# Kernel tuning notes

Measured on AMD Instinct MI355X. Metric: run time of the kernel, lower is better.

Reference implementation:

```python
import jax, jax.numpy as jnp
import numpy as np

BS, L, D, H, DC = 8, 8192, 128, 128, 128
C_CONST = 8.0  # rg-lru temperature constant


def _ln(x):
    # LayerNorm without scale/bias (use_bias=False, use_scale=False)
    m = jnp.mean(x, axis=-1, keepdims=True)
    v = jnp.mean(jnp.square(x - m), axis=-1, keepdims=True)
    return (x - m) * jax.lax.rsqrt(v + 1e-6)


def _affine(c, w, b):
    # Dense(features=1)(c)[:, :, None] -> (bs, 1, 1) broadcast scalar per sequence
    return (c @ w + b)[:, :, None]


def _combine(e1, e2):
    a1, b1 = e1
    a2, b2 = e2
    return (a1 * a2, a2 * b1 + b2)


def _linear_scan(a, b, reverse):
    # h_t = a_t * h_{t-1} + b_t (or h_{t+1} when reverse) along seq axis 1
    _, h = jax.lax.associative_scan(_combine, (a, b), axis=1, reverse=reverse)
    return h


def _forward(x, c, cln1_sw, cln1_sb, cln1_bw, cln1_bb, gate1_w, gate1_b,
             rnn_in_w, rnn_in_b, pos_emb, rnn_wi, rnn_bi, rnn_wr, rnn_br, rnn_a,
             rnn_out_w, rnn_out_b, cln2_sw, cln2_sb, cln2_bw, cln2_bb,
             gate2_w, gate2_b, mlp_w1, mlp_b1, mlp_w2, mlp_b2):
    # --- branch 1: conditioned LN -> bidirectional RG-LRU -> gated residual ---
    h = (1.0 + _affine(c, cln1_sw, cln1_sb)) * _ln(x) + _affine(c, cln1_bw, cln1_bb)
    u = _ln(h) @ rnn_in_w + rnn_in_b + pos_emb[None]          # (bs, L, H)
    gi = jax.nn.sigmoid(u @ rnn_wi + rnn_bi)                   # input gate
    gr = jax.nn.sigmoid(u @ rnn_wr + rnn_br)                   # recurrence gate
    at = jnp.exp(C_CONST * gr * jnp.log(rnn_a))                # a_t = a^(c*r_t)
    bt = jnp.sqrt(1.0 - jnp.square(at)) * (gi * u)
    hf = _linear_scan(at, bt, reverse=False)
    hb = _linear_scan(at, bt, reverse=True)
    r = jnp.concatenate([hf, hb], axis=-1) @ rnn_out_w + rnn_out_b  # (bs, L, D)
    x = x + _affine(c, gate1_w, gate1_b) * r
    # --- branch 2: conditioned LN -> gelu MLP -> gated residual ---
    h = (1.0 + _affine(c, cln2_sw, cln2_sb)) * _ln(x) + _affine(c, cln2_bw, cln2_bb)
    m = jax.nn.gelu(h @ mlp_w1 + mlp_b1) @ mlp_w2 + mlp_b2
    return x + _affine(c, gate2_w, gate2_b) * m


def setup_inputs() -> dict:
    key = jax.random.key(0)
    ks = jax.random.split(key, 30)
    def n(k, shape, s=0.05):
        return (jax.random.normal(k, shape) * s).astype(jnp.float32)
    rnn_a = (0.9 + 0.09 * jax.random.uniform(ks[0], (H,))).astype(jnp.float32)
    return {
        "x": jax.random.normal(ks[1], (BS, L, D), jnp.float32),
        "c": jax.random.normal(ks[2], (BS, DC), jnp.float32),
        "cln1_sw": n(ks[3], (DC, 1)), "cln1_sb": n(ks[4], (1,)),
        "cln1_bw": n(ks[5], (DC, 1)), "cln1_bb": n(ks[6], (1,)),
        "gate1_w": n(ks[7], (DC, 1)), "gate1_b": n(ks[8], (1,)),
        "rnn_in_w": n(ks[9], (D, H), 0.1), "rnn_in_b": n(ks[10], (H,)),
        "pos_emb": n(ks[11], (L, H), 0.02),
        "rnn_wi": n(ks[12], (H, H), 0.1), "rnn_bi": n(ks[13], (H,)),
        "rnn_wr": n(ks[14], (H, H), 0.1), "rnn_br": n(ks[15], (H,)),
        "rnn_a": rnn_a,
        "rnn_out_w": n(ks[16], (2 * H, D), 0.1), "rnn_out_b": n(ks[17], (D,)),
        "cln2_sw": n(ks[18], (DC, 1)), "cln2_sb": n(ks[19], (1,)),
        "cln2_bw": n(ks[20], (DC, 1)), "cln2_bb": n(ks[21], (1,)),
        "gate2_w": n(ks[22], (DC, 1)), "gate2_b": n(ks[23], (1,)),
        "mlp_w1": n(ks[24], (D, 4 * D), 0.1), "mlp_b1": n(ks[25], (4 * D,)),
        "mlp_w2": n(ks[26], (4 * D, D), 0.1), "mlp_b2": n(ks[27], (D,)),
    }


def reference(x, c, cln1_sw, cln1_sb, cln1_bw, cln1_bb, gate1_w, gate1_b,
              rnn_in_w, rnn_in_b, pos_emb, rnn_wi, rnn_bi, rnn_wr, rnn_br, rnn_a,
              rnn_out_w, rnn_out_b, cln2_sw, cln2_sb, cln2_bw, cln2_bb,
              gate2_w, gate2_b, mlp_w1, mlp_b1, mlp_w2, mlp_b2):
    return _forward(x, c, cln1_sw, cln1_sb, cln1_bw, cln1_bb, gate1_w, gate1_b,
                    rnn_in_w, rnn_in_b, pos_emb, rnn_wi, rnn_bi, rnn_wr, rnn_br, rnn_a,
                    rnn_out_w, rnn_out_b, cln2_sw, cln2_sb, cln2_bw, cln2_bb,
                    gate2_w, gate2_b, mlp_w1, mlp_b1, mlp_w2, mlp_b2)
```

## Files before the change

kernel.cpp:

```cpp
#include <hip/hip_runtime.h>
#include <hip/hip_bf16.h>

#define BSZ 8
#define SEQ 8192
#define DIM 128
#define NCH 128
#define CLEN 64

typedef unsigned short u16;
typedef unsigned int u32;
typedef short bf16x8 __attribute__((ext_vector_type(8)));
typedef float f32x4  __attribute__((ext_vector_type(4)));

__device__ __forceinline__ float us2f(u16 w){ union{u32 i;float f;}u; u.i=((u32)w)<<16; return u.f; }
__device__ __forceinline__ u16 f2us(float f){
  __hip_bfloat16 h = __float2bfloat16(f);
  union{ __hip_bfloat16 b; u16 s; }u; u.b=h; return u.s;
}
__device__ __forceinline__ float wred64(float v){
  #pragma unroll
  for (int o=1;o<64;o<<=1) v += __shfl_xor(v,o,64);
  return v;
}
__device__ __forceinline__ float red16(float v){
  v += __shfl_xor(v,1,64); v += __shfl_xor(v,2,64);
  v += __shfl_xor(v,4,64); v += __shfl_xor(v,8,64);
  return v;
}
__device__ __forceinline__ float sigmoidf_(float z){ return 1.f/(1.f+__expf(-z)); }
__device__ __forceinline__ float gelu_tanh(float x){
  float y = 0.7978845608028654f * fmaf(0.044715f*x, x*x, x);
  float e = __expf(2.f*y);
  float th = 1.f - 2.f/(e+1.f);
  return 0.5f*x*(1.f+th);
}
__device__ __forceinline__ void lds_fence(){
  asm volatile("s_waitcnt lgkmcnt(0)" ::: "memory");
  __builtin_amdgcn_sched_barrier(0);
}

__global__ __launch_bounds__(64) void k_aff(
    const float* __restrict__ c,
    const float* w0,const float* w1,const float* w2,const float* w3,const float* w4,const float* w5,
    const float* s0,const float* s1,const float* s2,const float* s3,const float* s4,const float* s5,
    float* __restrict__ aff)
{
  const float* ws[6]={w0,w1,w2,w3,w4,w5};
  const float* bs[6]={s0,s1,s2,s3,s4,s5};
  int l = threadIdx.x;
  for (int b=0;b<BSZ;++b){
    #pragma unroll
    for (int h=0;h<6;++h){
      float v = c[b*128+l]*ws[h][l] + c[b*128+64+l]*ws[h][64+l];
      v = wred64(v);
      if (l==0) aff[b*6+h] = v + bs[h][0];
    }
  }
}

__device__ __forceinline__ void pack_one(const float* __restrict__ W, int N,
                                         u16* __restrict__ out, int fi)
{
  int lane = fi & 63;
  int k2   = (fi >> 6) & 1;
  int cn   = fi >> 7;
  int NB   = N >> 4;
  int n    = cn % NB, c = cn / NB;
  int k0   = c*64 + k2*32 + (lane>>4)*8;
  int col  = n*16 + (lane&15);
  u16* o = out + (size_t)fi*8;
  #pragma unroll
  for (int j=0;j<8;++j) o[j] = f2us(W[(size_t)(k0+j)*N + col]);
}

__global__ __launch_bounds__(256) void k_prep(
    const float* __restrict__ w1, const float* __restrict__ w2, const float* __restrict__ wo,
    const float* __restrict__ win, const float* __restrict__ wi, const float* __restrict__ wr,
    u16* __restrict__ w1t, u16* __restrict__ w2t, u16* __restrict__ wot,
    u16* __restrict__ wint, u16* __restrict__ wit, u16* __restrict__ wrt)
{
  int i = blockIdx.x*256 + threadIdx.x;
  if      (i <  8192) pack_one(w1, 512, w1t, i);
  else if (i < 16384) pack_one(w2, 128, w2t, i-8192);
  else if (i < 20480) pack_one(wo, 128, wot, i-16384);
  else if (i < 22528) pack_one(win,128, wint,i-20480);
  else if (i < 24576) pack_one(wi, 128, wit, i-22528);
  else                pack_one(wr, 128, wrt, i-24576);
}

__global__ __launch_bounds__(256,4) void k_pre(
    const float* __restrict__ xg, const u16* __restrict__ wint, const float* __restrict__ b_in,
    const float* __restrict__ pos, const u16* __restrict__ wit, const float* __restrict__ b_i,
    const u16* __restrict__ wrt, const float* __restrict__ b_r, const float* __restrict__ avec,
    const float* __restrict__ aff,
    u32* __restrict__ abg,
    float* __restrict__ Ag, float* __restrict__ Bfg, float* __restrict__ Bbg)
{
  __shared__ __align__(16) u32 abp[CLEN*DIM];
  u16* A_l = (u16*)abp;
  const int t  = threadIdx.x;
  const int b  = blockIdx.x >> 7;
  const int ck = blockIdx.x & (NCH-1);
  const size_t base = ((size_t)(b*SEQ + ck*CLEN))*DIM;
  const int lane=t&63, wv=t>>6, col=lane&15, quad=lane>>4;
  const int m0 = wv*16;

  {
    const float s1p = 1.f + aff[b*6+0];
    const int cg=t&15, rg=t>>4, j0=cg*8, r0=rg*4;
    #pragma unroll
    for (int ii=0;ii<4;++ii){
      int r=r0+ii;
      const float* xo = xg + base + (size_t)r*DIM + j0;
      float4 a = *(const float4*)xo;
      float4 bq = *(const float4*)(xo+4);
      float o[8]={a.x,a.y,a.z,a.w,bq.x,bq.y,bq.z,bq.w};
      float s=0.f;
      #pragma unroll
      for (int j=0;j<8;++j) s+=o[j];
      s=red16(s); float m=s*(1.f/128.f);
      float q2=0.f;
      #pragma unroll
      for (int j=0;j<8;++j){ float d=o[j]-m; q2+=d*d; }
      q2=red16(q2); float var=q2*(1.f/128.f);
      float rs=rsqrtf(var+1e-6f);
      float vz=var*rs*rs;
      float tt2=s1p*rsqrtf(fmaf(s1p*s1p,vz,1e-6f));
      float sc=rs*tt2;
      u32 pk[4];
      #pragma unroll
      for (int q=0;q<4;++q){
        pk[q]= (u32)f2us((o[2*q]-m)*sc) | ((u32)f2us((o[2*q+1]-m)*sc)<<16);
      }
      *(uint4*)&A_l[r*136+j0] = make_uint4(pk[0],pk[1],pk[2],pk[3]);
    }
  }
  lds_fence();

  f32x4 uacc[8];
  #pragma unroll
  for (int n=0;n<8;++n) uacc[n]=(f32x4){0.f,0.f,0.f,0.f};
  #pragma unroll
  for (int c=0;c<2;++c){
    #pragma unroll
    for (int k2=0;k2<2;++k2){
      bf16x8 av = *(const bf16x8*)&A_l[(m0+col)*136 + c*64 + k2*32 + quad*8];
      #pragma unroll
      for (int n=0;n<8;++n){
        bf16x8 bv = *(const bf16x8*)&wint[(size_t)(((c*8+n)*2+k2)*64+lane)*8];
        uacc[n] = __builtin_amdgcn_mfma_f32_16x16x32_bf16(av, bv, uacc[n], 0,0,0);
      }
    }
  }
  float u_c[8][4];
  #pragma unroll
  for (int n=0;n<8;++n){
    int nc = n*16 + col;
    float bi = b_in[nc];
    #pragma unroll
    for (int r=0;r<4;++r){
      int row = m0 + quad*4 + r;
      u_c[n][r] = uacc[n][r] + bi + pos[(size_t)(ck*CLEN+row)*DIM + nc];
    }
  }
  #pragma unroll
  for (int n=0;n<8;++n){
    #pragma unroll
    for (int r=0;r<4;++r)
      A_l[(m0+quad*4+r)*136 + n*16+col] = f2us(u_c[n][r]);
  }
  lds_fence();

  f32x4 gacc[8], racc[8];
  #pragma unroll
  for (int n=0;n<8;++n){ gacc[n]=(f32x4){0.f,0.f,0.f,0.f}; racc[n]=(f32x4){0.f,0.f,0.f,0.f}; }
  #pragma unroll
  for (int c=0;c<2;++c){
    #pragma unroll
    for (int k2=0;k2<2;++k2){
      bf16x8 av = *(const bf16x8*)&A_l[(m0+col)*136 + c*64 + k2*32 + quad*8];
      #pragma unroll
      for (int n=0;n<8;++n){
        bf16x8 bgi = *(const bf16x8*)&wit[(size_t)(((c*8+n)*2+k2)*64+lane)*8];
        gacc[n] = __builtin_amdgcn_mfma_f32_16x16x32_bf16(av, bgi, gacc[n], 0,0,0);
        bf16x8 bgr = *(const bf16x8*)&wrt[(size_t)(((c*8+n)*2+k2)*64+lane)*8];
        racc[n] = __builtin_amdgcn_mfma_f32_16x16x32_bf16(av, bgr, racc[n], 0,0,0);
      }
    }
  }
  __syncthreads();

  #pragma unroll
  for (int n=0;n<8;++n){
    int nc = n*16 + col;
    float la = __logf(avec[nc]);
    float br = b_r[nc];
    float bi = b_i[nc];
    #pragma unroll
    for (int r=0;r<4;++r){
      int row = m0 + quad*4 + r;
      float gi = sigmoidf_(gacc[n][r]+bi);
      float g  = sigmoidf_(racc[n][r]+br);
      float a  = __expf(8.f*g*la);
      float bb = sqrtf(fmaxf(1.f-a*a,0.f))*gi*u_c[n][r];
      abp[row*DIM+nc] = (u32)f2us(a) | ((u32)f2us(bb)<<16);
    }
  }
  __syncthreads();

  {
    uint4* dst = (uint4*)(abg + base);
    const uint4* src = (const uint4*)abp;
    #pragma unroll
    for (int i=t;i<2048;i+=256) dst[i]=src[i];
  }

  const int sbase = (b*NCH+ck)*DIM;
  if (t < 128){
    float h=0.f, p=1.f;
    #pragma unroll 4
    for (int tt=0;tt<CLEN;++tt){
      u32 v=abp[tt*DIM+t];
      float a=us2f((u16)v), bb=us2f((u16)(v>>16));
      h=fmaf(a,h,bb); p*=a;
    }
    Ag[sbase+t]=p; Bfg[sbase+t]=h;
  } else {
    int ch=t-128; float h=0.f;
    #pragma unroll 4
    for (int tt=CLEN-1;tt>=0;--tt){
      u32 v=abp[tt*DIM+ch];
      h=fmaf(us2f((u16)v),h,us2f((u16)(v>>16)));
    }
    Bbg[sbase+ch]=h;
  }
}

__global__ __launch_bounds__(1024) void k_chunkscan(
    const float* __restrict__ Ag, const float* __restrict__ Bfg, const float* __restrict__ Bbg,
    float* __restrict__ Hf, float* __restrict__ Hb)
{
  __shared__ float sP[8][128], sS[8][128];
  const int dir = blockIdx.x >> 3, b = blockIdx.x & 7;
  const int t = threadIdx.x, seg = t>>7, ch = t&127;
  const size_t cbase = (size_t)b*NCH*DIM + ch;
  float P=1.f, S=0.f;
  if (dir==0){
    #pragma unroll 4
    for (int j=0;j<16;++j){
      size_t i = cbase + (size_t)(seg*16+j)*DIM;
      float a=Ag[i]; S=fmaf(a,S,Bfg[i]); P*=a;
    }
  } else {
    #pragma unroll 4
    for (int j=15;j>=0;--j){
      size_t i = cbase + (size_t)(seg*16+j)*DIM;
      float a=Ag[i]; S=fmaf(a,S,Bbg[i]); P*=a;
    }
  }
  sP[seg][ch]=P; sS[seg][ch]=S;
  __syncthreads();
  float h=0.f;
  if (dir==0){ for (int s=0;s<seg;++s) h=fmaf(sP[s][ch],h,sS[s][ch]); }
  else       { for (int s=7;s>seg;--s) h=fmaf(sP[s][ch],h,sS[s][ch]); }
  if (dir==0){
    #pragma unroll 4
    for (int j=0;j<16;++j){
      size_t i = cbase + (size_t)(seg*16+j)*DIM;
      Hf[i]=h; h=fmaf(Ag[i],h,Bfg[i]);
    }
  } else {
    #pragma unroll 4
    for (int j=15;j>=0;--j){
      size_t i = cbase + (size_t)(seg*16+j)*DIM;
      Hb[i]=h; h=fmaf(Ag[i],h,Bbg[i]);
    }
  }
}

__global__ __launch_bounds__(256,4) void k_scan(
    const u32* __restrict__ abg,
    const float* __restrict__ Hf, const float* __restrict__ Hb,
    const float* __restrict__ xg, const u16* __restrict__ wot, const float* __restrict__ b_out,
    const float* __restrict__ aff, float* __restrict__ outg)
{
  __shared__ __align__(16) u16 hcat[CLEN*264];
  const int t  = threadIdx.x;
  const int b  = blockIdx.x >> 7;
  const int ck = blockIdx.x & (NCH-1);
  const size_t base = ((size_t)(b*SEQ + ck*CLEN))*DIM;
  const int pbase=(b*NCH+ck)*DIM;

  if (t<128){
    const u32* p = abg + base + t;
    float h = Hf[pbase+t];
    u32 v0=p[0], v1=p[128], v2=p[256], v3=p[384];
    #pragma unroll
    for (int g=0; g<16; ++g){
      u32 n0=0,n1=0,n2=0,n3=0;
      if (g<15){
        n0=p[(g*4+4)*128]; n1=p[(g*4+5)*128];
        n2=p[(g*4+6)*128]; n3=p[(g*4+7)*128];
      }
      h=fmaf(us2f((u16)v0),h,us2f((u16)(v0>>16))); hcat[(g*4+0)*264+t]=f2us(h);
      h=fmaf(us2f((u16)v1),h,us2f((u16)(v1>>16))); hcat[(g*4+1)*264+t]=f2us(h);
      h=fmaf(us2f((u16)v2),h,us2f((u16)(v2>>16))); hcat[(g*4+2)*264+t]=f2us(h);
      h=fmaf(us2f((u16)v3),h,us2f((u16)(v3>>16))); hcat[(g*4+3)*264+t]=f2us(h);
      v0=n0; v1=n1; v2=n2; v3=n3;
    }
  } else {
    int ch=t-128;
    const u32* p = abg + base + ch;
    float h = Hb[pbase+ch];
    u32 v0=p[63*128], v1=p[62*128], v2=p[61*128], v3=p[60*128];
    #pragma unroll
    for (int g=0; g<16; ++g){
      u32 n0=0,n1=0,n2=0,n3=0;
      if (g<15){
        n0=p[(59-g*4)*128]; n1=p[(58-g*4)*128];
        n2=p[(57-g*4)*128]; n3=p[(56-g*4)*128];
      }
      h=fmaf(us2f((u16)v0),h,us2f((u16)(v0>>16))); hcat[(63-g*4)*264+128+ch]=f2us(h);
      h=fmaf(us2f((u16)v1),h,us2f((u16)(v1>>16))); hcat[(62-g*4)*264+128+ch]=f2us(h);
      h=fmaf(us2f((u16)v2),h,us2f((u16)(v2>>16))); hcat[(61-g*4)*264+128+ch]=f2us(h);
      h=fmaf(us2f((u16)v3),h,us2f((u16)(v3>>16))); hcat[(60-g*4)*264+128+ch]=f2us(h);
      v0=n0; v1=n1; v2=n2; v3=n3;
    }
  }
  __syncthreads();

  const int lane=t&63, wv=t>>6, col=lane&15, quad=lane>>4;
  const int m0 = wv*16;
  f32x4 acc[8];
  #pragma unroll
  for (int n=0;n<8;++n) acc[n]=(f32x4){0.f,0.f,0.f,0.f};
  #pragma unroll
  for (int chk=0; chk<4; ++chk){
    #pragma unroll
    for (int k2=0;k2<2;++k2){
      bf16x8 av = *(const bf16x8*)&hcat[(m0+col)*264 + chk*64 + k2*32 + quad*8];
      #pragma unroll
      for (int n=0;n<8;++n){
        bf16x8 bv = *(const bf16x8*)&wot[(size_t)(((chk*8+n)*2+k2)*64+lane)*8];
        acc[n] = __builtin_amdgcn_mfma_f32_16x16x32_bf16(av, bv, acc[n], 0,0,0);
      }
    }
  }
  __syncthreads();
  float* pbuf = (float*)hcat;
  #pragma unroll
  for (int n=0;n<8;++n){
    #pragma unroll
    for (int r=0;r<4;++r)
      pbuf[(m0+quad*4+r)*128 + n*16+col] = acc[n][r];
  }
  __syncthreads();

  const float g1=aff[b*6+2];
  const float4* xv4 = (const float4*)(xg+base);
  float4* ov4 = (float4*)(outg+base);
  const float4* cv4 = (const float4*)pbuf;
  #pragma unroll
  for (int i=t;i<2048;i+=256){
    float4 cv = cv4[i];
    float4 xv = xv4[i];
    float4 bo = *(const float4*)&b_out[(i*4)&127];
    float4 r;
    r.x=fmaf(g1,cv.x+bo.x,xv.x); r.y=fmaf(g1,cv.y+bo.y,xv.y);
    r.z=fmaf(g1,cv.z+bo.z,xv.z); r.w=fmaf(g1,cv.w+bo.w,xv.w);
    ov4[i]=r;
  }
}

__global__ __launch_bounds__(256,2) void k_mlp(
    const u16* __restrict__ w1t, const float* __restrict__ b1v,
    const u16* __restrict__ w2t, const float* __restrict__ b2v,
    const float* __restrict__ aff, float* __restrict__ outg)
{
  __shared__ u16 smem[CLEN*136 + 4*2*16*136];
  u16* h2l = smem;
  u16* m1t = smem + CLEN*136;
  const int t=threadIdx.x;
  const int b=blockIdx.x>>7;
  const size_t base=(size_t)blockIdx.x*CLEN*DIM;
  const int lane=t&63, wv=t>>6, col=lane&15, quad=lane>>4;
  const float s2p=1.f+aff[b*6+3], b2a=aff[b*6+4], g2=aff[b*6+5];
  u16* mw = m1t + wv*(2*16*136);

  {
    const int cg=t&15, rg=t>>4, j0=cg*8, r0=rg*4;
    #pragma unroll
    for (int ii=0;ii<4;++ii){
      int r=r0+ii;
      const float* xo = outg + base + (size_t)r*DIM + j0;
      float4 a = *(const float4*)xo;
      float4 bq = *(const float4*)(xo+4);
      float o[8]={a.x,a.y,a.z,a.w,bq.x,bq.y,bq.z,bq.w};
      float s=0.f;
      #pragma unroll
      for (int j=0;j<8;++j) s+=o[j];
      s=red16(s); float m=s*(1.f/128.f);
      float q2=0.f;
      #pragma unroll
      for (int j=0;j<8;++j){ float d=o[j]-m; q2+=d*d; }
      q2=red16(q2); float rs=rsqrtf(q2*(1.f/128.f)+1e-6f);
      u32 pk[4];
      #pragma unroll
      for (int q=0;q<4;++q){
        float a0=fmaf((o[2*q]-m)*rs,   s2p, b2a);
        float a1=fmaf((o[2*q+1]-m)*rs, s2p, b2a);
        pk[q]= (u32)f2us(a0) | ((u32)f2us(a1)<<16);
      }
      *(uint4*)&h2l[r*136+j0] = make_uint4(pk[0],pk[1],pk[2],pk[3]);
    }
  }
  __syncthreads();

  f32x4 acc2[4][8];
  #pragma unroll
  for (int m=0;m<4;++m)
    #pragma unroll
    for (int n=0;n<8;++n) acc2[m][n]=(f32x4){0.f,0.f,0.f,0.f};

  #pragma unroll
  for (int mp=0;mp<2;++mp){
    #pragma unroll
    for (int h=0;h<2;++h){
      f32x4 a1[2][4];
      #pragma unroll
      for (int m=0;m<2;++m)
        #pragma unroll
        for (int n=0;n<4;++n) a1[m][n]=(f32x4){0.f,0.f,0.f,0.f};
      #pragma unroll
      for (int c=0;c<2;++c){
        #pragma unroll
        for (int k2=0;k2<2;++k2){
          bf16x8 av0 = *(const bf16x8*)&h2l[((2*mp+0)*16+col)*136 + c*64 + k2*32 + quad*8];
          bf16x8 av1 = *(const bf16x8*)&h2l[((2*mp+1)*16+col)*136 + c*64 + k2*32 + quad*8];
          #pragma unroll
          for (int n=0;n<4;++n){
            int ng = wv*8 + h*4 + n;
            bf16x8 bv = *(const bf16x8*)&w1t[(size_t)(((c*32+ng)*2+k2)*64+lane)*8];
            a1[0][n] = __builtin_amdgcn_mfma_f32_16x16x32_bf16(av0, bv, a1[0][n], 0,0,0);
            a1[1][n] = __builtin_amdgcn_mfma_f32_16x16x32_bf16(av1, bv, a1[1][n], 0,0,0);
          }
        }
      }
      lds_fence();
      #pragma unroll
      for (int m=0;m<2;++m){
        #pragma unroll
        for (int n=0;n<4;++n){
          int lc = (h*4+n)*16 + col;
          float bb = b1v[wv*128 + lc];
          #pragma unroll
          for (int r=0;r<4;++r)
            mw[m*(16*136) + (quad*4+r)*136 + lc] = f2us(gelu_tanh(a1[m][n][r] + bb));
        }
      }
    }
    lds_fence();
    #pragma unroll
    for (int c2=0;c2<2;++c2){
      #pragma unroll
      for (int k2=0;k2<2;++k2){
        bf16x8 av0 = *(const bf16x8*)&mw[0*(16*136) + col*136 + c2*64 + k2*32 + quad*8];
        bf16x8 av1 = *(const bf16x8*)&mw[1*(16*136) + col*136 + c2*64 + k2*32 + quad*8];
        int cg = wv*2 + c2;
        #pragma unroll
        for (int n=0;n<8;++n){
          bf16x8 bv = *(const bf16x8*)&w2t[(size_t)(((cg*8+n)*2+k2)*64+lane)*8];
          acc2[2*mp+0][n] = __builtin_amdgcn_mfma_f32_16x16x32_bf16(av0, bv, acc2[2*mp+0][n], 0,0,0);
          acc2[2*mp+1][n] = __builtin_amdgcn_mfma_f32_16x16x32_bf16(av1, bv, acc2[2*mp+1][n], 0,0,0);
        }
      }
    }
  }
  __syncthreads();

  float* pbuf = (float*)smem;
  const int lrow = (lane>>4);
  const int cb   = (lane&15)*8;
  #pragma unroll
  for (int rt=0;rt<4;++rt){
    if (rt) __syncthreads();
    #pragma unroll
    for (int n=0;n<8;++n){
      #pragma unroll
      for (int r=0;r<4;++r)
        pbuf[wv*2048 + (quad*4+r)*128 + n*16+col] = acc2[rt][n][r];
    }
    __syncthreads();
    float s[8] = {0.f,0.f,0.f,0.f,0.f,0.f,0.f,0.f};
    #pragma unroll
    for (int p=0;p<4;++p){
      float4 x0 = *(const float4*)&pbuf[p*2048 + (4*wv+lrow)*128 + cb];
      float4 x1 = *(const float4*)&pbuf[p*2048 + (4*wv+lrow)*128 + cb + 4];
      s[0]+=x0.x; s[1]+=x0.y; s[2]+=x0.z; s[3]+=x0.w;
      s[4]+=x1.x; s[5]+=x1.y; s[6]+=x1.z; s[7]+=x1.w;
    }
    int grow = rt*16 + 4*wv + lrow;
    size_t gi = base + (size_t)grow*DIM + cb;
    float4 o0 = *(const float4*)&outg[gi];
    float4 o1 = *(const float4*)&outg[gi+4];
    float4 bb0 = *(const float4*)&b2v[cb];
    float4 bb1 = *(const float4*)&b2v[cb+4];
    float4 r0, r1;
    r0.x = fmaf(g2, s[0]+bb0.x, o0.x); r0.y = fmaf(g2, s[1]+bb0.y, o0.y);
    r0.z = fmaf(g2, s[2]+bb0.z, o0.z); r0.w = fmaf(g2, s[3]+bb0.w, o0.w);
    r1.x = fmaf(g2, s[4]+bb1.x, o1.x); r1.y = fmaf(g2, s[5]+bb1.y, o1.y);
    r1.z = fmaf(g2, s[6]+bb1.z, o1.z); r1.w = fmaf(g2, s[7]+bb1.w, o1.w);
    *(float4*)&outg[gi]   = r0;
    *(float4*)&outg[gi+4] = r1;
  }
}

extern "C" void kernel_launch(void* const* d_in, const int* in_sizes, int n_in,
                              void* d_out, int out_size, void* d_ws, size_t ws_size,
                              hipStream_t stream)
{
  (void)in_sizes; (void)n_in; (void)out_size; (void)ws_size;
  const float* x   =(const float*)d_in[0];
  const float* c   =(const float*)d_in[1];
  const float* c1sw=(const float*)d_in[2];  const float* c1sb=(const float*)d_in[3];
  const float* c1bw=(const float*)d_in[4];  const float* c1bb=(const float*)d_in[5];
  const float* g1w =(const float*)d_in[6];  const float* g1b =(const float*)d_in[7];
  const float* win =(const float*)d_in[8];  const float* binv=(const float*)d_in[9];
  const float* pos =(const float*)d_in[10];
  const float* wi  =(const float*)d_in[11]; const float* biv =(const float*)d_in[12];
  const float* wr  =(const float*)d_in[13]; const float* brv =(const float*)d_in[14];
  const float* av  =(const float*)d_in[15];
  const float* wout=(const float*)d_in[16]; const float* bout=(const float*)d_in[17];
  const float* c2sw=(const float*)d_in[18]; const float* c2sb=(const float*)d_in[19];
  const float* c2bw=(const float*)d_in[20]; const float* c2bb=(const float*)d_in[21];
  const float* g2w =(const float*)d_in[22]; const float* g2b =(const float*)d_in[23];
  const float* w1  =(const float*)d_in[24]; const float* b1v =(const float*)d_in[25];
  const float* w2  =(const float*)d_in[26]; const float* b2v =(const float*)d_in[27];

  float* wsf  = (float*)d_ws;
  float* Ag   = wsf;
  float* Bfg  = Ag   + 131072;
  float* Bbg  = Bfg  + 131072;
  float* Hf   = Bbg  + 131072;
  float* Hb   = Hf   + 131072;
  float* aff  = Hb   + 131072;
  u16*   w1t  = (u16*)(aff + 64);
  u16*   w2t  = w1t + 65536;
  u16*   wot  = w2t + 65536;
  u16*   wint = wot + 32768;
  u16*   wit  = wint + 16384;
  u16*   wrt  = wit  + 16384;
  u32*   abg  = (u32*)(wrt + 16384);

  float* outg = (float*)d_out;

  k_aff<<<dim3(1),dim3(64),0,stream>>>(c, c1sw,c1bw,g1w,c2sw,c2bw,g2w,
                                       c1sb,c1bb,g1b,c2sb,c2bb,g2b, aff);
  k_prep<<<dim3(104),dim3(256),0,stream>>>(w1,w2,wout,win,wi,wr,
                                           w1t,w2t,wot,wint,wit,wrt);
  k_pre<<<dim3(BSZ*NCH),dim3(256),0,stream>>>(x,wint,binv,pos,wit,biv,wrt,brv,av,aff,
                                              abg, Ag,Bfg,Bbg);
  k_chunkscan<<<dim3(16),dim3(1024),0,stream>>>(Ag,Bfg,Bbg,Hf,Hb);
  k_scan<<<dim3(BSZ*NCH),dim3(256),0,stream>>>(abg,Hf,Hb,x,wot,bout,aff,outg);
  k_mlp<<<dim3(BSZ*NCH),dim3(256),0,stream>>>(w1t,b1v,w2t,b2v,aff,outg);
}
```

Before: 271.1 us.

## Keep MLP hidden activations in registers via transposed MFMA and bpermute

Restructures the MLP kernel's first GEMM into a transposed form (weights as A operand, activations as B), so the GELU outputs already sit in a register layout close to what the second GEMM needs. Lanes exchange them with ds_bpermute instead of writing them to LDS and reading them back. This drops the per-wave LDS scratch region and its fences, shrinking shared memory, which may allow more occupancy. In exchange it adds many bpermute instructions and selects per step, and it changes the loop order and register pressure.

```diff
diff --git a/kernel.cpp b/kernel.cpp
--- a/kernel.cpp
+++ b/kernel.cpp
@@ -377,15 +377,15 @@
     const u16* __restrict__ w2t, const float* __restrict__ b2v,
     const float* __restrict__ aff, float* __restrict__ outg)
 {
-  __shared__ u16 smem[CLEN*136 + 4*2*16*136];
-  u16* h2l = smem;
-  u16* m1t = smem + CLEN*136;
+  __shared__ __align__(16) u32 smem4[8192];
+  u16* h2l = (u16*)smem4;
   const int t=threadIdx.x;
   const int b=blockIdx.x>>7;
   const size_t base=(size_t)blockIdx.x*CLEN*DIM;
   const int lane=t&63, wv=t>>6, col=lane&15, quad=lane>>4;
   const float s2p=1.f+aff[b*6+3], b2a=aff[b*6+4], g2=aff[b*6+5];
-  u16* mw = m1t + wv*(2*16*136);
+  const int idx01 = (((lane>>4)&1)*32 + (lane&15))*4;
+  const int idx23 = idx01 + 64;
 
   {
     const int cg=t&15, rg=t>>4, j0=cg*8, r0=rg*4;
@@ -422,63 +422,66 @@
     #pragma unroll
     for (int n=0;n<8;++n) acc2[m][n]=(f32x4){0.f,0.f,0.f,0.f};
 
-  #pragma unroll
-  for (int mp=0;mp<2;++mp){
-    #pragma unroll
-    for (int h=0;h<2;++h){
-      f32x4 a1[2][4];
-      #pragma unroll
-      for (int m=0;m<2;++m)
-        #pragma unroll
-        for (int n=0;n<4;++n) a1[m][n]=(f32x4){0.f,0.f,0.f,0.f};
-      #pragma unroll
-      for (int c=0;c<2;++c){
-        #pragma unroll
-        for (int k2=0;k2<2;++k2){
-          bf16x8 av0 = *(const bf16x8*)&h2l[((2*mp+0)*16+col)*136 + c*64 + k2*32 + quad*8];
-          bf16x8 av1 = *(const bf16x8*)&h2l[((2*mp+1)*16+col)*136 + c*64 + k2*32 + quad*8];
-          #pragma unroll
-          for (int n=0;n<4;++n){
-            int ng = wv*8 + h*4 + n;
-            bf16x8 bv = *(const bf16x8*)&w1t[(size_t)(((c*32+ng)*2+k2)*64+lane)*8];
-            a1[0][n] = __builtin_amdgcn_mfma_f32_16x16x32_bf16(av0, bv, a1[0][n], 0,0,0);
-            a1[1][n] = __builtin_amdgcn_mfma_f32_16x16x32_bf16(av1, bv, a1[1][n], 0,0,0);
-          }
-        }
-      }
-      lds_fence();
-      #pragma unroll
-      for (int m=0;m<2;++m){
-        #pragma unroll
-        for (int n=0;n<4;++n){
-          int lc = (h*4+n)*16 + col;
-          float bb = b1v[wv*128 + lc];
-          #pragma unroll
-          for (int r=0;r<4;++r)
-            mw[m*(16*136) + (quad*4+r)*136 + lc] = f2us(gelu_tanh(a1[m][n][r] + bb));
-        }
-      }
-    }
-    lds_fence();
-    #pragma unroll
-    for (int c2=0;c2<2;++c2){
-      #pragma unroll
-      for (int k2=0;k2<2;++k2){
-        bf16x8 av0 = *(const bf16x8*)&mw[0*(16*136) + col*136 + c2*64 + k2*32 + quad*8];
-        bf16x8 av1 = *(const bf16x8*)&mw[1*(16*136) + col*136 + c2*64 + k2*32 + quad*8];
-        int cg = wv*2 + c2;
-        #pragma unroll
-        for (int n=0;n<8;++n){
-          bf16x8 bv = *(const bf16x8*)&w2t[(size_t)(((cg*8+n)*2+k2)*64+lane)*8];
-          acc2[2*mp+0][n] = __builtin_amdgcn_mfma_f32_16x16x32_bf16(av0, bv, acc2[2*mp+0][n], 0,0,0);
-          acc2[2*mp+1][n] = __builtin_amdgcn_mfma_f32_16x16x32_bf16(av1, bv, acc2[2*mp+1][n], 0,0,0);
-        }
-      }
-    }
-  }
-  __syncthreads();
-
-  float* pbuf = (float*)smem;
+  for (int s=0;s<4;++s){
+    f32x4 ap[2][4];
+    #pragma unroll
+    for (int nt=0;nt<2;++nt)
+      #pragma unroll
+      for (int mt=0;mt<4;++mt) ap[nt][mt]=(f32x4){0.f,0.f,0.f,0.f};
+    #pragma unroll
+    for (int kk=0;kk<4;++kk){
+      bf16x8 a0 = *(const bf16x8*)&w1t[((size_t)(((kk>>1)*32 + (wv*8 + 2*s+0))*2 + (kk&1))*64 + lane)*8];
+      bf16x8 a1 = *(const bf16x8*)&w1t[((size_t)(((kk>>1)*32 + (wv*8 + 2*s+1))*2 + (kk&1))*64 + lane)*8];
+      #pragma unroll
+      for (int mt=0;mt<4;++mt){
+        bf16x8 bq = *(const bf16x8*)&h2l[(mt*16+col)*136 + kk*32 + quad*8];
+        ap[0][mt] = __builtin_amdgcn_mfma_f32_16x16x32_bf16(a0, bq, ap[0][mt], 0,0,0);
+        ap[1][mt] = __builtin_amdgcn_mfma_f32_16x16x32_bf16(a1, bq, ap[1][mt], 0,0,0);
+      }
+    }
+    float4 b1q0 = *(const float4*)&b1v[wv*128 + (2*s+0)*16 + quad*4];
+    float4 b1q1 = *(const float4*)&b1v[wv*128 + (2*s+1)*16 + quad*4];
+    u32 lo0[4], hi0[4], lo1[4], hi1[4];
+    #pragma unroll
+    for (int mt=0;mt<4;++mt){
+      float g0=gelu_tanh(ap[0][mt][0]+b1q0.x), g1=gelu_tanh(ap[0][mt][1]+b1q0.y);
+      float g2_=gelu_tanh(ap[0][mt][2]+b1q0.z), g3=gelu_tanh(ap[0][mt][3]+b1q0.w);
+      lo0[mt]=(u32)f2us(g0)|((u32)f2us(g1)<<16);
+      hi0[mt]=(u32)f2us(g2_)|((u32)f2us(g3)<<16);
+      float h0=gelu_tanh(ap[1][mt][0]+b1q1.x), h1=gelu_tanh(ap[1][mt][1]+b1q1.y);
+      float h2_=gelu_tanh(ap[1][mt][2]+b1q1.z), h3=gelu_tanh(ap[1][mt][3]+b1q1.w);
+      lo1[mt]=(u32)f2us(h0)|((u32)f2us(h1)<<16);
+      hi1[mt]=(u32)f2us(h2_)|((u32)f2us(h3)<<16);
+    }
+    union F8 { bf16x8 v; u32 u[4]; } m1f[4];
+    const bool hiq = (lane & 32) != 0;
+    #pragma unroll
+    for (int mt=0;mt<4;++mt){
+      u32 pa, pb;
+      pa=(u32)__builtin_amdgcn_ds_bpermute(idx01,(int)lo0[mt]);
+      pb=(u32)__builtin_amdgcn_ds_bpermute(idx01,(int)lo1[mt]);
+      m1f[mt].u[0] = hiq ? pb : pa;
+      pa=(u32)__builtin_amdgcn_ds_bpermute(idx01,(int)hi0[mt]);
+      pb=(u32)__builtin_amdgcn_ds_bpermute(idx01,(int)hi1[mt]);
+      m1f[mt].u[1] = hiq ? pb : pa;
+      pa=(u32)__builtin_amdgcn_ds_bpermute(idx23,(int)lo0[mt]);
+      pb=(u32)__builtin_amdgcn_ds_bpermute(idx23,(int)lo1[mt]);
+      m1f[mt].u[2] = hiq ? pb : pa;
+      pa=(u32)__builtin_amdgcn_ds_bpermute(idx23,(int)hi0[mt]);
+      pb=(u32)__builtin_amdgcn_ds_bpermute(idx23,(int)hi1[mt]);
+      m1f[mt].u[3] = hiq ? pb : pa;
+    }
+    #pragma unroll
+    for (int n2=0;n2<8;++n2){
+      bf16x8 bw = *(const bf16x8*)&w2t[((size_t)(((wv*2+(s>>1))*8 + n2)*2 + (s&1))*64 + lane)*8];
+      #pragma unroll
+      for (int mt=0;mt<4;++mt)
+        acc2[mt][n2] = __builtin_amdgcn_mfma_f32_16x16x32_bf16(m1f[mt].v, bw, acc2[mt][n2], 0,0,0);
+    }
+  }
+  __syncthreads();
+
+  float* pbuf = (float*)smem4;
   const int lrow = (lane>>4);
   const int cb   = (lane&15)*8;
   #pragma unroll
```

Result: slower. 278.5 us (+2.8%).

## Switch MLP to 32x32x16 MFMA with register-resident GELU intermediate via permlane swap

Applied to the files above, without the earlier changes.

Rewrites the MLP kernel to use 32x32x16 bf16 MFMA instead of 16x16x32, with repacked w1/w2 fragment layouts. The first GEMM computes the transposed hidden tile, so after GELU the results are rearranged across lane halves with v_permlane32_swap and fed straight into the second GEMM as A operands. This removes the LDS round trip and fences for the hidden activations and shrinks shared memory. The price is a new weight packing layout, inline asm that is specific to gfx950, and different register pressure.

```diff
diff --git a/kernel.cpp b/kernel.cpp
--- a/kernel.cpp
+++ b/kernel.cpp
@@ -11,6 +11,7 @@
 typedef unsigned int u32;
 typedef short bf16x8 __attribute__((ext_vector_type(8)));
 typedef float f32x4  __attribute__((ext_vector_type(4)));
+typedef float f32x16 __attribute__((ext_vector_type(16)));
 
 __device__ __forceinline__ float us2f(u16 w){ union{u32 i;float f;}u; u.i=((u32)w)<<16; return u.f; }
 __device__ __forceinline__ u16 f2us(float f){
@@ -73,6 +74,32 @@
   for (int j=0;j<8;++j) o[j] = f2us(W[(size_t)(k0+j)*N + col]);
 }
 
+__device__ __forceinline__ void pack32A(const float* __restrict__ W, int N,
+                                        u16* __restrict__ out, int fi)
+{
+  int lane = fi & 63;
+  int ks   = (fi >> 6) & 7;
+  int ng   = fi >> 9;
+  int k0   = ks*16 + (lane>>5)*8;
+  int col  = ng*32 + (lane&31);
+  u16* o = out + (size_t)fi*8;
+  #pragma unroll
+  for (int j=0;j<8;++j) o[j] = f2us(W[(size_t)(k0+j)*N + col]);
+}
+
+__device__ __forceinline__ void pack32B(const float* __restrict__ W, int N,
+                                        u16* __restrict__ out, int fi)
+{
+  int lane = fi & 63;
+  int ot   = (fi >> 6) & 3;
+  int ksg  = fi >> 8;
+  int k0   = ksg*16 + (lane>>5)*8;
+  int col  = ot*32 + (lane&31);
+  u16* o = out + (size_t)fi*8;
+  #pragma unroll
+  for (int j=0;j<8;++j) o[j] = f2us(W[(size_t)(k0+j)*N + col]);
+}
+
 __global__ __launch_bounds__(256) void k_prep(
     const float* __restrict__ w1, const float* __restrict__ w2, const float* __restrict__ wo,
     const float* __restrict__ win, const float* __restrict__ wi, const float* __restrict__ wr,
@@ -80,8 +107,8 @@
     u16* __restrict__ wint, u16* __restrict__ wit, u16* __restrict__ wrt)
 {
   int i = blockIdx.x*256 + threadIdx.x;
-  if      (i <  8192) pack_one(w1, 512, w1t, i);
-  else if (i < 16384) pack_one(w2, 128, w2t, i-8192);
+  if      (i <  8192) pack32A(w1, 512, w1t, i);
+  else if (i < 16384) pack32B(w2, 128, w2t, i-8192);
   else if (i < 20480) pack_one(wo, 128, wot, i-16384);
   else if (i < 22528) pack_one(win,128, wint,i-20480);
   else if (i < 24576) pack_one(wi, 128, wit, i-22528);
@@ -377,15 +404,14 @@
     const u16* __restrict__ w2t, const float* __restrict__ b2v,
     const float* __restrict__ aff, float* __restrict__ outg)
 {
-  __shared__ u16 smem[CLEN*136 + 4*2*16*136];
-  u16* h2l = smem;
-  u16* m1t = smem + CLEN*136;
+  __shared__ __align__(16) u32 smem4[8192];
+  u16* h2l = (u16*)smem4;
   const int t=threadIdx.x;
   const int b=blockIdx.x>>7;
   const size_t base=(size_t)blockIdx.x*CLEN*DIM;
-  const int lane=t&63, wv=t>>6, col=lane&15, quad=lane>>4;
+  const int lane=t&63, wv=t>>6;
+  const int l31=lane&31, h5=lane>>5;
   const float s2p=1.f+aff[b*6+3], b2a=aff[b*6+4], g2=aff[b*6+5];
-  u16* mw = m1t + wv*(2*16*136);
 
   {
     const int cg=t&15, rg=t>>4, j0=cg*8, r0=rg*4;
@@ -416,79 +442,76 @@
   }
   __syncthreads();
 
-  f32x4 acc2[4][8];
-  #pragma unroll
-  for (int m=0;m<4;++m)
-    #pragma unroll
-    for (int n=0;n<8;++n) acc2[m][n]=(f32x4){0.f,0.f,0.f,0.f};
-
-  #pragma unroll
-  for (int mp=0;mp<2;++mp){
-    #pragma unroll
-    for (int h=0;h<2;++h){
-      f32x4 a1[2][4];
-      #pragma unroll
-      for (int m=0;m<2;++m)
+  f32x16 acc2[2][4];
+  #pragma unroll
+  for (int m=0;m<2;++m)
+    #pragma unroll
+    for (int n=0;n<4;++n)
+      #pragma unroll
+      for (int r=0;r<16;++r) acc2[m][n][r]=0.f;
+
+  for (int nt=0;nt<4;++nt){
+    bf16x8 w1A[8];
+    #pragma unroll
+    for (int ks=0;ks<8;++ks)
+      w1A[ks] = *(const bf16x8*)&w1t[((size_t)((wv*4+nt)*8 + ks)*64 + lane)*8];
+    #pragma unroll
+    for (int tt=0;tt<2;++tt){
+      f32x16 a1;
+      #pragma unroll
+      for (int r=0;r<16;++r) a1[r]=0.f;
+      #pragma unroll
+      for (int ks=0;ks<8;++ks){
+        bf16x8 hb = *(const bf16x8*)&h2l[(tt*32 + l31)*136 + ks*16 + h5*8];
+        a1 = __builtin_amdgcn_mfma_f32_32x32x16_bf16(w1A[ks], hb, a1, 0,0,0);
+      }
+      u32 pk[8];
+      #pragma unroll
+      for (int q=0;q<4;++q){
+        float4 bq = *(const float4*)&b1v[wv*128 + nt*32 + q*8 + h5*4];
+        float g0=gelu_tanh(a1[4*q+0]+bq.x);
+        float g1=gelu_tanh(a1[4*q+1]+bq.y);
+        float g2_=gelu_tanh(a1[4*q+2]+bq.z);
+        float g3=gelu_tanh(a1[4*q+3]+bq.w);
+        pk[2*q+0]=(u32)f2us(g0)|((u32)f2us(g1)<<16);
+        pk[2*q+1]=(u32)f2us(g2_)|((u32)f2us(g3)<<16);
+      }
+      asm volatile("v_permlane32_swap_b32 %0, %1" : "+v"(pk[0]), "+v"(pk[2]));
+      asm volatile("v_permlane32_swap_b32 %0, %1" : "+v"(pk[1]), "+v"(pk[3]));
+      asm volatile("v_permlane32_swap_b32 %0, %1" : "+v"(pk[4]), "+v"(pk[6]));
+      asm volatile("v_permlane32_swap_b32 %0, %1" : "+v"(pk[5]), "+v"(pk[7]));
+      union F8 { bf16x8 v; u32 u[4]; } A0, A1;
+      A0.u[0]=pk[0]; A0.u[1]=pk[1]; A0.u[2]=pk[2]; A0.u[3]=pk[3];
+      A1.u[0]=pk[4]; A1.u[1]=pk[5]; A1.u[2]=pk[6]; A1.u[3]=pk[7];
+      #pragma unroll
+      for (int ot=0;ot<4;++ot){
+        bf16x8 wb0 = *(const bf16x8*)&w2t[((size_t)((wv*8 + nt*2 + 0)*4 + ot)*64 + lane)*8];
+        acc2[tt][ot] = __builtin_amdgcn_mfma_f32_32x32x16_bf16(A0.v, wb0, acc2[tt][ot], 0,0,0);
+        bf16x8 wb1 = *(const bf16x8*)&w2t[((size_t)((wv*8 + nt*2 + 1)*4 + ot)*64 + lane)*8];
+        acc2[tt][ot] = __builtin_amdgcn_mfma_f32_32x32x16_bf16(A1.v, wb1, acc2[tt][ot], 0,0,0);
+      }
+    }
+  }
+  __syncthreads();
+
+  float* pbuf = (float*)smem4;
+  const int lrow = (lane>>4)&3;
+  const int cb   = (lane&15)*8;
+  #pragma unroll
+  for (int rt=0;rt<4;++rt){
+    const int tt = rt>>1, gg = rt&1;
+    if (rt) __syncthreads();
+    #pragma unroll
+    for (int ot=0;ot<4;++ot){
+      #pragma unroll
+      for (int q=0;q<2;++q){
         #pragma unroll
-        for (int n=0;n<4;++n) a1[m][n]=(f32x4){0.f,0.f,0.f,0.f};
-      #pragma unroll
-      for (int c=0;c<2;++c){
-        #pragma unroll
-        for (int k2=0;k2<2;++k2){
-          bf16x8 av0 = *(const bf16x8*)&h2l[((2*mp+0)*16+col)*136 + c*64 + k2*32 + quad*8];
-          bf16x8 av1 = *(const bf16x8*)&h2l[((2*mp+1)*16+col)*136 + c*64 + k2*32 + quad*8];
-          #pragma unroll
-          for (int n=0;n<4;++n){
-            int ng = wv*8 + h*4 + n;
-            bf16x8 bv = *(const bf16x8*)&w1t[(size_t)(((c*32+ng)*2+k2)*64+lane)*8];
-            a1[0][n] = __builtin_amdgcn_mfma_f32_16x16x32_bf16(av0, bv, a1[0][n], 0,0,0);
-            a1[1][n] = __builtin_amdgcn_mfma_f32_16x16x32_bf16(av1, bv, a1[1][n], 0,0,0);
-          }
+        for (int r=0;r<4;++r){
+          int reg = gg*8 + q*4 + r;
+          int tl  = q*8 + r + 4*h5;
+          pbuf[wv*2048 + tl*128 + ot*32 + l31] = acc2[tt][ot][reg];
         }
       }
-      lds_fence();
-      #pragma unroll
-      for (int m=0;m<2;++m){
-        #pragma unroll
-        for (int n=0;n<4;++n){
-          int lc = (h*4+n)*16 + col;
-          float bb = b1v[wv*128 + lc];
-          #pragma unroll
-          for (int r=0;r<4;++r)
-            mw[m*(16*136) + (quad*4+r)*136 + lc] = f2us(gelu_tanh(a1[m][n][r] + bb));
-        }
-      }
-    }
-    lds_fence();
-    #pragma unroll
-    for (int c2=0;c2<2;++c2){
-      #pragma unroll
-      for (int k2=0;k2<2;++k2){
-        bf16x8 av0 = *(const bf16x8*)&mw[0*(16*136) + col*136 + c2*64 + k2*32 + quad*8];
-        bf16x8 av1 = *(const bf16x8*)&mw[1*(16*136) + col*136 + c2*64 + k2*32 + quad*8];
-        int cg = wv*2 + c2;
-        #pragma unroll
-        for (int n=0;n<8;++n){
-          bf16x8 bv = *(const bf16x8*)&w2t[(size_t)(((cg*8+n)*2+k2)*64+lane)*8];
-          acc2[2*mp+0][n] = __builtin_amdgcn_mfma_f32_16x16x32_bf16(av0, bv, acc2[2*mp+0][n], 0,0,0);
-          acc2[2*mp+1][n] = __builtin_amdgcn_mfma_f32_16x16x32_bf16(av1, bv, acc2[2*mp+1][n], 0,0,0);
-        }
-      }
-    }
-  }
-  __syncthreads();
-
-  float* pbuf = (float*)smem;
-  const int lrow = (lane>>4);
-  const int cb   = (lane&15)*8;
-  #pragma unroll
-  for (int rt=0;rt<4;++rt){
-    if (rt) __syncthreads();
-    #pragma unroll
-    for (int n=0;n<8;++n){
-      #pragma unroll
-      for (int r=0;r<4;++r)
-        pbuf[wv*2048 + (quad*4+r)*128 + n*16+col] = acc2[rt][n][r];
     }
     __syncthreads();
     float s[8] = {0.f,0.f,0.f,0.f,0.f,0.f,0.f,0.f};
```

After: 272.6 us. Within noise of the previous version (+0.6%).
